# Optimization experiments

Measured on AMD Instinct MI355X. Metric: run time of the kernel, lower is better.

The kernel has to match this reference:

```python
import jax, jax.numpy as jnp
import numpy as np


def setup_inputs() -> dict:
    key = jax.random.key(0)
    ks = jax.random.split(key, 32)
    B, S, H, E, Vs, T = 32, 400, 512, 300, 200, 32
    EN, V = 50000, 50200
    rn = lambda k, shape, s=0.05: jax.random.normal(k, shape, jnp.float32) * s
    return {
        'encoder_hidden': rn(ks[0], (B, S, 2 * H), 1.0),
        'hidden0': rn(ks[1], (B, H), 1.0),
        'user_embed': rn(ks[2], (B, E), 1.0),
        'W_embed': rn(ks[3], (EN, E), 1.0),
        'W_ih': rn(ks[4], (3 * H, E)), 'W_hh': rn(ks[5], (3 * H, H)),
        'b_ih': rn(ks[6], (3 * H,)), 'b_hh': rn(ks[7], (3 * H,)),
        'Wk_c': rn(ks[8], (2 * H, H)), 'bk_c': rn(ks[9], (H,)),
        'Wq_c': rn(ks[10], (H, H)), 'bq_c': rn(ks[11], (H,)),
        'we_c': rn(ks[12], (H,)), 'be_c': rn(ks[13], (1,)),
        'Wk_u': rn(ks[14], (E, H)), 'bk_u': rn(ks[15], (H,)),
        'Wq_u': rn(ks[16], (H, H)), 'bq_u': rn(ks[17], (H,)),
        'we_u': rn(ks[18], (H,)), 'be_u': rn(ks[19], (1,)),
        'Wc': rn(ks[20], (3 * H + 2 * E, H)),
        'Wg': rn(ks[21], (3 * H + E,)), 'bg': rn(ks[22], (1,)),
        'Wgen': rn(ks[23], (H, EN)),
        'src_mask': jnp.ones((B, S), jnp.int32),
        'tgt_': jax.random.randint(ks[24], (B, T), 0, EN),
        'specific_vocab': jax.random.randint(ks[25], (B, Vs), 0, EN),
        'vocab_size': V,
    }


def reference(encoder_hidden, hidden0, user_embed, W_embed, W_ih, W_hh, b_ih, b_hh,
              Wk_c, bk_c, Wq_c, bq_c, we_c, be_c, Wk_u, bk_u, Wq_u, bq_u, we_u, be_u,
              Wc, Wg, bg, Wgen, src_mask, tgt_, specific_vocab, vocab_size):
    B, T = tgt_.shape
    # teacher forcing: prev token embed, step 0 uses <s> token id 1
    tgt_embed = W_embed[tgt_]                                  # [B,T,E]
    init_embed = jnp.broadcast_to(W_embed[1], (B, 1, W_embed.shape[1]))
    prev = jnp.concatenate([init_embed, tgt_embed[:, :T - 1]], axis=1)
    xs = jnp.swapaxes(prev, 0, 1)                              # [T,B,E]

    user_vocab_emb = W_embed[specific_vocab]                   # [B,Vs,E]
    proj_key_c = encoder_hidden @ Wk_c + bk_c                  # [B,S,H]
    proj_key_u = user_vocab_emb @ Wk_u + bk_u                  # [B,Vs,H]
    mask = src_mask != 0
    batch_idx = jnp.arange(B)[:, None]

    def gru_cell(h, x):
        gi = x @ W_ih.T + b_ih
        gh = h @ W_hh.T + b_hh
        i_r, i_z, i_n = jnp.split(gi, 3, axis=-1)
        h_r, h_z, h_n = jnp.split(gh, 3, axis=-1)
        r = jax.nn.sigmoid(i_r + h_r)
        z = jax.nn.sigmoid(i_z + h_z)
        n = jnp.tanh(i_n + r * h_n)
        return (1.0 - z) * n + z * h

    def step(h, x):
        h = gru_cell(h, x)                                     # [B,H]
        q = h
        # Bahdanau attention over encoder states
        sc = jnp.tanh((q @ Wq_c + bq_c)[:, None, :] + proj_key_c) @ we_c + be_c  # [B,S]
        sc = jnp.where(mask, sc, -1e9)
        ac = jax.nn.softmax(sc, axis=-1)
        ctx_c = jnp.einsum('bs,bsd->bd', ac, encoder_hidden)   # [B,2H]
        # Bahdanau attention over user-specific vocab embeddings
        su = jnp.tanh((q @ Wq_u + bq_u)[:, None, :] + proj_key_u) @ we_u + be_u  # [B,Vs]
        au = jax.nn.softmax(su, axis=-1)
        ctx_u = jnp.einsum('bv,bve->be', au, user_vocab_emb)   # [B,E]
        ch = jnp.tanh(jnp.concatenate([q, ctx_c, ctx_u, user_embed], axis=-1) @ Wc)
        gen_prob = jax.nn.softmax(ch @ Wgen, axis=-1)          # [B,embed_num]
        gen_prob = jnp.pad(gen_prob, ((0, 0), (0, vocab_size - gen_prob.shape[-1])))
        copy_prob = jnp.zeros((B, vocab_size), gen_prob.dtype).at[batch_idx, specific_vocab].add(au)
        copy_p = jax.nn.sigmoid(jnp.concatenate([ctx_c, q, ctx_u], axis=-1) @ Wg + bg[0])[:, None]
        mix = copy_p * copy_prob + (1.0 - copy_p) * gen_prob   # [B,vocab]
        return h, mix

    _, probs = jax.lax.scan(step, hidden0, xs)                 # [T,B,V]
    return jnp.swapaxes(probs, 0, 1)                           # [B,T,V]
```

## Files before the change

### kernel.cpp

```cpp
#include <hip/hip_runtime.h>


typedef __attribute__((ext_vector_type(8))) short short8;
typedef __attribute__((ext_vector_type(4))) float f32x4;
typedef unsigned short us;

#define SCW (-2.8853900817779268f)

__device__ __forceinline__ float bf2f(us u) {
  return __uint_as_float(((unsigned)u) << 16);
}
__device__ __forceinline__ us f2bf(float f) {
  unsigned x = __float_as_uint(f);
  unsigned r = x + 0x7fffu + ((x >> 16) & 1u);
  return (us)(r >> 16);
}
__device__ __forceinline__ float fsigmoid(float x) { return 1.f / (1.f + __expf(-x)); }
__device__ __forceinline__ float ftanh(float x) {
  float t = __expf(-2.f * fabsf(x));
  float r = (1.f - t) / (1.f + t);
  return x >= 0.f ? r : -r;
}
__device__ __forceinline__ float ftanh_fast(float x) {
  float u = exp2f(SCW * fabsf(x));
  float r = (1.f - u) * __builtin_amdgcn_rcpf(1.f + u);
  return copysignf(r, x);
}

struct PP {
  const float *enc, *hidden0, *Wk_c, *Wk_u, *Wq_c, *Wq_u, *Wc, *W_ih, *W_hh, *W_embed;
  const int *tgt, *sv;
  us *encb, *hball, *WkcT, *WkuT, *WqcuT, *WcT, *WihT, *WhhF, *xe, *uve;
};

__device__ void tcast_job(const float* __restrict__ src, us* __restrict__ dst,
                          int R, int C, int Rpad, int x, int y, float scale,
                          int lt, float* tb) {
  int tx = lt & 31, ty = lt >> 5;
  int c0 = x * 32, r0 = y * 32;
#pragma unroll
  for (int i = 0; i < 4; ++i) {
    int r = r0 + ty + i * 8, c = c0 + tx;
    tb[(ty + i * 8) * 33 + tx] = (r < R && c < C) ? src[(size_t)r * C + c] : 0.f;
  }
  __syncthreads();
#pragma unroll
  for (int i = 0; i < 4; ++i) {
    int c = c0 + ty + i * 8, rr = r0 + tx;
    if (c < C && rr < Rpad)
      dst[(size_t)c * Rpad + rr] = f2bf(scale * tb[tx * 33 + ty + i * 8]);
  }
}

__global__ __launch_bounds__(256) void k_prep(PP P) {
  __shared__ float tb[32 * 33];
  const int bid = blockIdx.x, tid = threadIdx.x;
  if (bid < 1024) {
    for (int i = bid * 256 + tid; i < 3276800; i += 1024 * 256) {
      float4 v = ((const float4*)P.enc)[i];
// ... 54 lines not shown
}

__global__ __launch_bounds__(256) void k_tcastX(const float* __restrict__ src0,
                                                us* __restrict__ dst0,
                                                int R, int C, int Rpad,
                                                size_t srcB, size_t dstB) {
  __shared__ float tile[32 * 33];
  const float* src = src0 + (size_t)blockIdx.z * srcB;
  us* dst = dst0 + (size_t)blockIdx.z * dstB;
  tcast_job(src, dst, R, C, Rpad, blockIdx.x, blockIdx.y, 1.f, threadIdx.x, tile);
}
__global__ __launch_bounds__(256) void k_tcastXb(const us* __restrict__ src0,
                                                 us* __restrict__ dst0,
                                                 int R, int C, int Rpad,
                                                 size_t srcB, size_t dstB) {
  __shared__ us tile[32][33];
  const us* src = src0 + (size_t)blockIdx.z * srcB;
  us* dst = dst0 + (size_t)blockIdx.z * dstB;
  int c0 = blockIdx.x * 32, r0 = blockIdx.y * 32;
  int tx = threadIdx.x & 31, ty = threadIdx.x >> 5;
#pragma unroll
  for (int i = 0; i < 4; ++i) {
    int r = r0 + ty + i * 8, c = c0 + tx;
    tile[ty + i * 8][tx] = (r < R && c < C) ? src[(size_t)r * C + c] : (us)0;
  }
  __syncthreads();
#pragma unroll
  for (int i = 0; i < 4; ++i) {
    int c = c0 + ty + i * 8, rr = r0 + tx;
    if (c < C && rr < Rpad) dst[(size_t)c * Rpad + rr] = tile[tx][ty + i * 8];
  }
}

template <int MODE>
__global__ __launch_bounds__(512) void gemm_bt(const us* __restrict__ A,
                                               const us* __restrict__ BT,
                                               int M, int N, int K, int Ntiles,
                                               const float* __restrict__ bias,
                                               float bscale,
                                               us* __restrict__ outB,
                                               float* __restrict__ outF,
                                               float* __restrict__ rowsum) {
  __shared__ us sh[12288];
  __shared__ float rs[256];
  us* As = sh;
  us* Bs = sh + 8192;
  const int tid = threadIdx.x;
  const int lane = tid & 63, wid = tid >> 6;
  const int wr = wid >> 1, wc = wid & 1;
  const int bx = blockIdx.x;
  const int mt = bx / Ntiles, nt = bx - mt * Ntiles;
  const int m0 = mt * 256, n0 = nt * 128;
  f32x4 acc[4][4] = {};
  for (int kk = 0; kk < K; kk += 32) {
    uint4 av0, av1, bv;
    {
      int c = tid, row = c >> 2, c8 = (c & 3) * 8;
      av0 = *(const uint4*)(A + (size_t)(m0 + row) * K + kk + c8);
      c = tid + 512; row = c >> 2; c8 = (c & 3) * 8;
      av1 = *(const uint4*)(A + (size_t)(m0 + row) * K + kk + c8);
      c = tid; row = c >> 2; c8 = (c & 3) * 8;
      int nr = n0 + row; if (nr > N - 1) nr = N - 1;
      bv = *(const uint4*)(BT + (size_t)nr * K + kk + c8);
    }
    __syncthreads();
    ((uint4*)As)[tid] = av0;
    ((uint4*)As)[tid + 512] = av1;
    ((uint4*)Bs)[tid] = bv;
    __syncthreads();
    short8 af[4], bfr[4];
#pragma unroll
    for (int m = 0; m < 4; ++m)
      af[m] = *(const short8*)(As + (wr * 64 + m * 16 + (lane & 15)) * 32 + (lane >> 4) * 8);
#pragma unroll
    for (int n = 0; n < 4; ++n)
      bfr[n] = *(const short8*)(Bs + (wc * 64 + n * 16 + (lane & 15)) * 32 + (lane >> 4) * 8);
#pragma unroll
    for (int m = 0; m < 4; ++m)
#pragma unroll
      for (int n = 0; n < 4; ++n)
        acc[m][n] = __builtin_amdgcn_mfma_f32_16x16x32_bf16(af[m], bfr[n], acc[m][n], 0, 0, 0);
  }
  if (MODE == 0) {
#pragma unroll
// ... 78 lines not shown
    ((uint4*)As)[tid] = av;
    ((uint4*)Bs)[tid * 2] = bv0;
    ((uint4*)Bs)[tid * 2 + 1] = bv1;
    __syncthreads();
    short8 af[4], bf0, bf1;
#pragma unroll
    for (int m = 0; m < 4; ++m)
      af[m] = *(const short8*)(As + (m * 16 + (lane & 15)) * 32 + (lane >> 4) * 8);
    bf0 = *(const short8*)(Bs + ((w * 2 + 0) * 16 + (lane & 15)) * 32 + (lane >> 4) * 8);
    bf1 = *(const short8*)(Bs + ((w * 2 + 1) * 16 + (lane & 15)) * 32 + (lane >> 4) * 8);
#pragma unroll
    for (int m = 0; m < 4; ++m) {
      acc[m][0] = __builtin_amdgcn_mfma_f32_16x16x32_bf16(af[m], bf0, acc[m][0], 0, 0, 0);
      acc[m][1] = __builtin_amdgcn_mfma_f32_16x16x32_bf16(af[m], bf1, acc[m][1], 0, 0, 0);
    }
  }
#pragma unroll
  for (int m = 0; m < 4; ++m)
#pragma unroll
    for (int q = 0; q < 2; ++q)
#pragma unroll
      for (int reg = 0; reg < 4; ++reg) {
        int r = m0 + m * 16 + (lane >> 4) * 4 + reg;
        int c = n0 + (w * 2 + q) * 16 + (lane & 15);
        float v = acc[m][q][reg];
        if (MODE == 0) v += bscale * bias[c];
        else v = ftanh_fast(v);
        outB[(size_t)r * N + c] = f2bf(v);
      }
}

struct FP {
  const us* frag; const us* gib; const float* bhh; const float* hidden0;
  us* hball; float* hfall; int* arrive;
  const us* xe; const us* WihT; const float* bih; us* gibout;
  const us* encb; const us* WkcT; const float* bkc; us* pkc;
  const us* uve; const us* WkuT; const float* bku; us* pku;
  const float* Wgen; us* WT;
  const float* enc; us* encTp;
  us* uveTp;
};

__device__ void gru_body(const FP& P, int q, int tid, char* pool) {
  us* hs = (us*)pool;
  float* gh = (float*)(pool + 32768);
  const int lane = tid & 63, w = tid >> 6;
  short8 bfr[16];
  {
    const us* fb = P.frag + (((size_t)(q * 12 + w) * 16) * 64 + lane) * 8;
#pragma unroll
    for (int kt = 0; kt < 16; ++kt) bfr[kt] = *(const short8*)(fb + (size_t)kt * 512);
  }
  float hprev[3];
#pragma unroll
  for (int s = 0; s < 3; ++s) {
    int i = tid + s * 768;
    if (i < 2048) {
      int b = i >> 6, jj = i & 63;
      hprev[s] = P.hidden0[b * 512 + q * 64 + jj];
    }
  }
  if (tid == 0) {
    while (__hip_atomic_load(P.arrive + 32, __ATOMIC_ACQUIRE,
                             __HIP_MEMORY_SCOPE_AGENT) < 48) {
      __builtin_amdgcn_s_sleep(1);
    }
  }
  __syncthreads();
  const int sw = (lane & 7) << 3;
  for (int t = 0; t < 32; ++t) {
    if (t > 0) {
      if (tid == 0) {
        while (__hip_atomic_load(P.arrive + (t - 1), __ATOMIC_ACQUIRE,
                                 __HIP_MEMORY_SCOPE_AGENT) < 8) {
          __builtin_amdgcn_s_sleep(1);
        }
      }
      __syncthreads();
    }
    const us* hp = P.hball + (size_t)t * 16384;
    for (int i = tid; i < 2048; i += 768)
      ((uint4*)hs)[i ^ ((i >> 6) & 7)] = *(const uint4*)(hp + i * 8);
    __syncthreads();
    f32x4 acc0 = {}, acc1 = {};
#pragma unroll
    for (int kt = 0; kt < 16; ++kt) {
      int base0 = ((lane & 15) * 512 + kt * 32 + (lane >> 4) * 8) ^ sw;
      int base1 = (((lane & 15) + 16) * 512 + kt * 32 + (lane >> 4) * 8) ^ sw;
      short8 a0 = *(const short8*)(hs + base0);
      short8 a1 = *(const short8*)(hs + base1);
      acc0 = __builtin_amdgcn_mfma_f32_16x16x32_bf16(a0, bfr[kt], acc0, 0, 0, 0);
      acc1 = __builtin_amdgcn_mfma_f32_16x16x32_bf16(a1, bfr[kt], acc1, 0, 0, 0);
    }
    {
      int col = w * 16 + (lane & 15);
#pragma unroll
      for (int reg = 0; reg < 4; ++reg) {
        gh[col * 33 + ((lane >> 4) * 4 + reg)] = acc0[reg];
        gh[col * 33 + (16 + (lane >> 4) * 4 + reg)] = acc1[reg];
      }
    }
    __syncthreads();
    us* hbn = P.hball + (size_t)(t + 1) * 16384;
    float* hfn = P.hfall + (size_t)t * 16384;
#pragma unroll
    for (int s = 0; s < 3; ++s) {
      int i = tid + s * 768;
      if (i < 2048) {
        int b = i >> 6, jj = i & 63, j = q * 64 + jj;
        float g0 = gh[jj * 33 + b] + P.bhh[j];
        float g1 = gh[(64 + jj) * 33 + b] + P.bhh[512 + j];
        float g2 = gh[(128 + jj) * 33 + b] + P.bhh[1024 + j];
        size_t gbase = (size_t)(t * 32 + b) * 1536;
        float r_ = fsigmoid(bf2f(P.gib[gbase + j]) + g0);
        float z_ = fsigmoid(bf2f(P.gib[gbase + 512 + j]) + g1);
        float n_ = ftanh(bf2f(P.gib[gbase + 1024 + j]) + r_ * g2);
        float hv = (1.f - z_) * n_ + z_ * hprev[s];
        hprev[s] = hv;
        hbn[b * 512 + j] = f2bf(hv);
        hfn[b * 512 + j] = hv;
      }
    }
    __syncthreads();
    if (tid == 0)
      __hip_atomic_fetch_add(P.arrive + t, 1, __ATOMIC_RELEASE,
                             __HIP_MEMORY_SCOPE_AGENT);
  }
}

__device__ void gemm0_body(const us* A, const us* BT, int N, int K,
                           int mt, int nt, const float* bias, float bscale,
                           us* outB, int tid, char* pool) {
  us* As = (us*)pool;
  us* Bs = (us*)(pool + 16384);
  const bool act = tid < 512;
  const int lane = tid & 63, wid = (tid >> 6) & 7;
  const int wr = wid >> 1, wc = wid & 1;
  const int m0 = mt * 256, n0 = nt * 128;
  f32x4 acc[4][4] = {};
  for (int kk = 0; kk < K; kk += 32) {
    uint4 av0 = {0, 0, 0, 0}, av1 = {0, 0, 0, 0}, bv = {0, 0, 0, 0};
    if (act) {
      int c = tid, row = c >> 2, c8 = (c & 3) * 8;
      av0 = *(const uint4*)(A + (size_t)(m0 + row) * K + kk + c8);
      av1 = *(const uint4*)(A + (size_t)(m0 + 128 + row) * K + kk + c8);
      int nr = n0 + row; if (nr > N - 1) nr = N - 1;
      bv = *(const uint4*)(BT + (size_t)nr * K + kk + c8);
    }
    __syncthreads();
    if (act) {
      ((uint4*)As)[tid] = av0;
      ((uint4*)As)[tid + 512] = av1;
      ((uint4*)Bs)[tid] = bv;
    }
    __syncthreads();
    if (act) {
      short8 af[4], bfr[4];
#pragma unroll
      for (int m = 0; m < 4; ++m)
        af[m] = *(const short8*)(As + (wr * 64 + m * 16 + (lane & 15)) * 32 + (lane >> 4) * 8);
#pragma unroll
      for (int n = 0; n < 4; ++n)
        bfr[n] = *(const short8*)(Bs + (wc * 64 + n * 16 + (lane & 15)) * 32 + (lane >> 4) * 8);
#pragma unroll
      for (int m = 0; m < 4; ++m)
#pragma unroll
        for (int n = 0; n < 4; ++n)
          acc[m][n] = __builtin_amdgcn_mfma_f32_16x16x32_bf16(af[m], bfr[n], acc[m][n], 0, 0, 0);
    }
  }
  if (act) {
#pragma unroll
    for (int m = 0; m < 4; ++m)
#pragma unroll
      for (int n = 0; n < 4; ++n)
#pragma unroll
        for (int reg = 0; reg < 4; ++reg) {
          int r = m0 + wr * 64 + m * 16 + (lane >> 4) * 4 + reg;
          int c = n0 + wc * 64 + n * 16 + (lane & 15);
          outB[(size_t)r * N + c] = f2bf(acc[m][n][reg] + bscale * bias[c]);
        }
  }
}

__global__ __launch_bounds__(768, 1) void k_fat(FP P) {
  __shared__ char pool[98304];
  const int bid = blockIdx.x, tid = threadIdx.x;
  if (bid < 8) { gru_body(P, bid, tid, pool); return; }
  if (bid < 56) {
    int j = bid - 8;
    gemm0_body(P.xe, P.WihT, 1536, 320, j / 12, j % 12, P.bih, 1.f, P.gibout, tid, pool);
    __syncthreads();
    if (tid == 0)
      __hip_atomic_fetch_add(P.arrive + 32, 1, __ATOMIC_RELEASE,
                             __HIP_MEMORY_SCOPE_AGENT);
    return;
  }
  if (bid < 256) {
    int j = bid - 56;
    gemm0_body(P.encb, P.WkcT, 512, 1024, j >> 2, j & 3, P.bkc, SCW, P.pkc, tid, pool);
    return;
  }
  if (bid < 356) {
    int j = bid - 256;
    gemm0_body(P.uve, P.WkuT, 512, 320, j >> 2, j & 3, P.bku, SCW, P.pku, tid, pool);
    return;
  }
  const int g = tid >> 8, lt = tid & 255;
  const int tx = lt & 31, ty = lt >> 5;
  float* tb = (float*)(pool + g * 4224);
  if (bid < 878) {
    int base = (bid - 356) * 3 + g;
    for (int it = 0; it < 16; ++it) {
      int sub = base + it * 1566;
      bool valid = sub < 25008;
      int x = valid ? sub % 1563 : 0, y = valid ? sub / 1563 : 0;
      int c0 = x * 32, r0 = y * 32;
      if (valid) {
#pragma unroll
        for (int i = 0; i < 4; ++i) {
          int r = r0 + ty + i * 8, c = c0 + tx;
          tb[(ty + i * 8) * 33 + tx] =
              (c < 50000) ? P.Wgen[(size_t)r * 50000 + c] : 0.f;
        }
      }
      __syncthreads();
      if (valid) {
#pragma unroll
        for (int i = 0; i < 4; ++i) {
          int c = c0 + ty + i * 8;
          if (c < 50000)
            P.WT[(size_t)c * 512 + r0 + tx] = f2bf(tb[tx * 33 + ty + i * 8]);
        }
      }
      __syncthreads();
    }
    return;
  }
  if (bid < 1156) {
    int base = (bid - 878) * 3 + g;
    for (int it = 0; it < 16; ++it) {
      int sub = base + it * 834;
      bool valid = sub < 13312;
      int x = sub & 31, rem = sub >> 5;
      int y = rem % 13, z = rem / 13;
      const float* src = P.enc + (size_t)z * 409600;
      us* dst = P.encTp + (size_t)z * 425984;
      int c0 = x * 32, r0 = y * 32;
      if (valid) {
#pragma unroll
        for (int i = 0; i < 4; ++i) {
          int r = r0 + ty + i * 8, c = c0 + tx;
          tb[(ty + i * 8) * 33 + tx] = (r < 400) ? src[(size_t)r * 1024 + c] : 0.f;
        }
      }
      __syncthreads();
      if (valid) {
#pragma unroll
        for (int i = 0; i < 4; ++i) {
          int c = c0 + ty + i * 8, rr = r0 + tx;
          if (rr < 416) dst[(size_t)c * 416 + rr] = f2bf(tb[tx * 33 + ty + i * 8]);
        }
      }
      __syncthreads();
    }
    return;
  }
  {
    us* tbu = (us*)tb;
    int base = (bid - 1156) * 3 + g;
    for (int it = 0; it < 16; ++it) {
      int sub = base + it * 141;
      bool valid = sub < 2240;
      int x = sub % 10, rem = sub / 10;
      int y = rem % 7, z = rem / 7;
      const us* src = P.uve + (size_t)z * 64000;
      us* dst = P.uveTp + (size_t)z * 71680;
      int c0 = x * 32, r0 = y * 32;
      if (valid) {
#pragma unroll
        for (int i = 0; i < 4; ++i) {
          int r = r0 + ty + i * 8, c = c0 + tx;
          tbu[(ty + i * 8) * 33 + tx] = (r < 200) ? src[(size_t)r * 320 + c] : (us)0;
        }
      }
      __syncthreads();
      if (valid) {
#pragma unroll
        for (int i = 0; i < 4; ++i) {
          int c = c0 + ty + i * 8, rr = r0 + tx;
          if (rr < 224) dst[(size_t)c * 224 + rr] = tbu[tx * 33 + ty + i * 8];
        }
      }
      __syncthreads();
    }
  }
}

__global__ __launch_bounds__(256) void k_scores(const us* __restrict__ Qall,
                                                const us* __restrict__ pkc,
                                                const us* __restrict__ pku,
                                                const float* __restrict__ wec,
                                                const float* __restrict__ bec,
// ... 11 lines not shown
    int r = bid % 50;
    s0 = (r >> 1) * 16; th = r & 1; qoff = 0; S = 400;
  } else {
    int j = bid - 1600;
    b = j / 26;
    int r = j % 26;
    s0 = (r >> 1) * 16; th = r & 1; qoff = 512; S = 200;
  }
  for (int i = threadIdx.x; i < 1024; i += 256) {
    int tt = th * 16 + (i >> 6), c8 = (i & 63) * 8;
    ((uint4*)q)[i] = *(const uint4*)(Qall + (size_t)(tt * 32 + b) * 1024 + qoff + c8);
  }
  const int w = threadIdx.x >> 6, lane = threadIdx.x & 63;
  const int d0 = lane * 8;
  const float* we = enc ? wec : weu;
  float wef[8];
  {
    float4 w0 = *(const float4*)(we + d0);
    float4 w1 = *(const float4*)(we + d0 + 4);
    wef[0] = w0.x; wef[1] = w0.y; wef[2] = w0.z; wef[3] = w0.w;
    wef[4] = w1.x; wef[5] = w1.y; wef[6] = w1.z; wef[7] = w1.w;
  }
  const float bias = enc ? bec[0] : beu[0];
  float pkf[4][8];
  int ss[4], validv[4], maskedv[4];
#pragma unroll
  for (int si = 0; si < 4; ++si) {
    int s = s0 + w * 4 + si;
    validv[si] = (s < S);
    int sc = validv[si] ? s : (S - 1);
    ss[si] = sc;
    const us* pk = enc ? pkc + ((size_t)b * 400 + sc) * 512
                       : pku + ((size_t)b * 200 + sc) * 512;
    uint4 pkv = *(const uint4*)(pk + d0);
    pkf[si][0] = bf2f((us)(pkv.x & 0xffff)); pkf[si][1] = bf2f((us)(pkv.x >> 16));
    pkf[si][2] = bf2f((us)(pkv.y & 0xffff)); pkf[si][3] = bf2f((us)(pkv.y >> 16));
    pkf[si][4] = bf2f((us)(pkv.z & 0xffff)); pkf[si][5] = bf2f((us)(pkv.z >> 16));
    pkf[si][6] = bf2f((us)(pkv.w & 0xffff)); pkf[si][7] = bf2f((us)(pkv.w >> 16));
    maskedv[si] = enc ? (src_mask[b * 400 + sc] == 0) : 0;
  }
  __syncthreads();
  for (int tl = 0; tl < 16; ++tl) {
    short8 qv = *(const short8*)(q + tl * 512 + d0);
    float qf[8];
#pragma unroll
    for (int d = 0; d < 8; ++d) qf[d] = bf2f((us)qv[d]);
#pragma unroll
    for (int si = 0; si < 4; ++si) {
      float a = 0.f;
#pragma unroll
      for (int d = 0; d < 8; ++d) {
        float x = qf[d] + pkf[si][d];
        float u = exp2f(-fabsf(x));
        float r2v = (1.f - u) * __builtin_amdgcn_rcpf(1.f + u);
        a = fmaf(copysignf(r2v, -x), wef[d], a);
      }
#pragma unroll
      for (int m = 1; m < 64; m <<= 1) a += __shfl_xor(a, m, 64);
      if (lane == 0 && validv[si]) {
        int t = th * 16 + tl;
        float v = a + bias;
        if (enc) sc_enc[(size_t)(t * 32 + b) * 400 + ss[si]] = maskedv[si] ? -1e9f : v;
        else sc_usr[(size_t)(t * 32 + b) * 200 + ss[si]] = v;
      }
    }
  }
}

__device__ __forceinline__ float bmax256(float v, float* r4, int tid) {
#pragma unroll
  for (int m = 1; m < 64; m <<= 1) v = fmaxf(v, __shfl_xor(v, m, 64));
  if ((tid & 63) == 0) r4[tid >> 6] = v;
  __syncthreads();
  float x = fmaxf(fmaxf(r4[0], r4[1]), fmaxf(r4[2], r4[3]));
  __syncthreads();
  return x;
}
__device__ __forceinline__ float bsum256(float v, float* r4, int tid) {
#pragma unroll
  for (int m = 1; m < 64; m <<= 1) v += __shfl_xor(v, m, 64);
  if ((tid & 63) == 0) r4[tid >> 6] = v;
  __syncthreads();
  float x = r4[0] + r4[1] + r4[2] + r4[3];
  __syncthreads();
  return x;
}

__global__ __launch_bounds__(256) void k_softmax(const float* __restrict__ sc_enc,
                                                 const float* __restrict__ sc_usr,
                                                 const float* __restrict__ bg,
                                                 us* __restrict__ AC,
                                                 us* __restrict__ AU,
                                                 float* __restrict__ aual,
                                                 float* __restrict__ cp_acc) {
  __shared__ float r4[4];
  int r = blockIdx.x, tid = threadIdx.x;
  if (r < 1024) {
    int t = r >> 5, b = r & 31;
    float v0 = (tid < 400) ? sc_enc[(size_t)r * 400 + tid] : -3e38f;
    float v1 = (tid + 256 < 400) ? sc_enc[(size_t)r * 400 + tid + 256] : -3e38f;
    float mx = bmax256(fmaxf(v0, v1), r4, tid);
    float e0 = (tid < 400) ? __expf(v0 - mx) : 0.f;
    float e1 = (tid + 256 < 400) ? __expf(v1 - mx) : 0.f;
    float inv = 1.f / bsum256(e0 + e1, r4, tid);
    us* ACb = AC + (size_t)(b * 32 + t) * 416;
    if (tid < 400) ACb[tid] = f2bf(e0 * inv);
    int s2 = tid + 256;
    if (s2 < 400) ACb[s2] = f2bf(e1 * inv);
    else if (s2 < 416) ACb[s2] = 0;
    if (tid == 0) cp_acc[r] = bg[0];
  } else {
    int rr = r - 1024;
    int t = rr >> 5, b = rr & 31;
    float v0 = (tid < 200) ? sc_usr[(size_t)rr * 200 + tid] : -3e38f;
    float mx = bmax256(v0, r4, tid);
    float e0 = (tid < 200) ? __expf(v0 - mx) : 0.f;
    float inv = 1.f / bsum256(e0, r4, tid);
    us* AUb = AU + (size_t)(b * 32 + t) * 224;
    if (tid < 200) {
      float a = e0 * inv;
      AUb[tid] = f2bf(a);
      aual[(size_t)rr * 200 + tid] = a;
    } else if (tid < 224) {
      AUb[tid] = 0;
    }
  }
}

__global__ __launch_bounds__(256) void k_ctx(const us* __restrict__ A,
                                             const us* __restrict__ BT,
                                             const float* __restrict__ Wg,
                                             us* __restrict__ catall,
                                             float* __restrict__ cp_acc,
                                             int N, int Kp, int catOff, int wgOff,
                                             int Nvalid) {
  __shared__ us As[32 * 32];
  __shared__ us Bs[128 * 32];
  __shared__ float gaccs[32];
  const int b = blockIdx.y, n0 = blockIdx.x * 128;
  const us* Ab = A + (size_t)b * 32 * Kp;
  const us* Bb = BT + (size_t)b * N * Kp;
  const int tid = threadIdx.x, lane = tid & 63, w = tid >> 6;
  if (tid < 32) gaccs[tid] = 0.f;
  f32x4 acc[2][2] = {};
  for (int kk = 0; kk < Kp; kk += 32) {
    uint4 av, bv0, bv1;
    if (tid < 128) av = *(const uint4*)(Ab + (size_t)(tid >> 2) * Kp + kk + (tid & 3) * 8);
    {
      int i0 = tid * 2, row0 = i0 >> 2, c0 = (i0 & 3) * 8;
      int i1 = tid * 2 + 1, row1 = i1 >> 2, c1 = (i1 & 3) * 8;
      int nr0 = n0 + row0; if (nr0 > N - 1) nr0 = N - 1;
      int nr1 = n0 + row1; if (nr1 > N - 1) nr1 = N - 1;
      bv0 = *(const uint4*)(Bb + (size_t)nr0 * Kp + kk + c0);
      bv1 = *(const uint4*)(Bb + (size_t)nr1 * Kp + kk + c1);
    }
    __syncthreads();
    if (tid < 128) ((uint4*)As)[tid] = av;
    ((uint4*)Bs)[tid * 2] = bv0;
    ((uint4*)Bs)[tid * 2 + 1] = bv1;
    __syncthreads();
    short8 a0 = *(const short8*)(As + ((lane & 15)) * 32 + (lane >> 4) * 8);
    short8 a1 = *(const short8*)(As + (16 + (lane & 15)) * 32 + (lane >> 4) * 8);
#pragma unroll
    for (int qq = 0; qq < 2; ++qq) {
      short8 bf_ = *(const short8*)(Bs + ((w * 2 + qq) * 16 + (lane & 15)) * 32 + (lane >> 4) * 8);
      acc[0][qq] = __builtin_amdgcn_mfma_f32_16x16x32_bf16(a0, bf_, acc[0][qq], 0, 0, 0);
      acc[1][qq] = __builtin_amdgcn_mfma_f32_16x16x32_bf16(a1, bf_, acc[1][qq], 0, 0, 0);
    }
  }
#pragma unroll
  for (int mt = 0; mt < 2; ++mt)
#pragma unroll
    for (int qq = 0; qq < 2; ++qq)
#pragma unroll
      for (int reg = 0; reg < 4; ++reg) {
        int t_ = mt * 16 + (lane >> 4) * 4 + reg;
        int c = n0 + (w * 2 + qq) * 16 + (lane & 15);
        if (c < Nvalid) {
          float v = acc[mt][qq][reg];
          catall[(size_t)(t_ * 32 + b) * 2144 + catOff + c] = f2bf(v);
          atomicAdd(&gaccs[t_], v * Wg[wgOff + c]);
        }
      }
  __syncthreads();
  if (tid < 32) atomicAdd(&cp_acc[tid * 32 + b], gaccs[tid]);
}

__global__ __launch_bounds__(256) void k_catgate(const us* __restrict__ hball,
                                                 const float* __restrict__ hfall,
                                                 const float* __restrict__ ue,
                                                 const float* __restrict__ Wg,
                                                 const float* __restrict__ cp_acc,
                                                 us* __restrict__ catall,
                                                 float* __restrict__ cp_all) {
  __shared__ float r4[4];
  int r = blockIdx.x, tid = threadIdx.x;
  int t = r >> 5, b = r & 31;
  us* row = catall + (size_t)r * 2144;
  const us* hb = hball + (size_t)(t + 1) * 16384 + b * 512;
  row[tid] = hb[tid];
  row[256 + tid] = hb[256 + tid];
  float gp = 0.f;
  for (int i = tid; i < 512; i += 256)
    gp += hfall[(size_t)t * 16384 + b * 512 + i] * Wg[1024 + i];
  for (int i = tid; i < 308; i += 256)
    row[1836 + i] = (i < 300) ? f2bf(ue[b * 300 + i]) : (us)0;
  float gtot = bsum256(gp, r4, tid);
  if (tid == 0) cp_all[r] = fsigmoid(gtot + cp_acc[r]);
}

__global__ __launch_bounds__(256) void k_finalize(float* __restrict__ out,
                                                  const float* __restrict__ rowsum,
                                                  const float* __restrict__ cp_all,
                                                  const float* __restrict__ au_all,
                                                  const int* __restrict__ sv) {
  int r = blockIdx.x;
  int t = threadIdx.x;
  int b = r & 31, tt = r >> 5;
  float cp = cp_all[r];
  float scale = (1.f - cp) / rowsum[r];
  float* base = out + (size_t)(b * 32 + tt) * 50200;
  float4* b4 = (float4*)base;
  for (int i = t; i < 12550; i += 256) {
    if (i < 12500) {
      float4 v = b4[i];
      v.x *= scale; v.y *= scale; v.z *= scale; v.w *= scale;
      b4[i] = v;
    } else {
      b4[i] = make_float4(0.f, 0.f, 0.f, 0.f);
    }
  }
  __syncthreads();
  if (t < 200) {
    int idx = sv[b * 200 + t];
    atomicAdd(base + idx, cp * au_all[(size_t)r * 200 + t]);
  }
}

__global__ __launch_bounds__(256) void k_finalize2(const us* __restrict__ expb,
                                                   const float* __restrict__ rowsum,
                                                   const float* __restrict__ cp_all,
                                                   const float* __restrict__ au_all,
                                                   const int* __restrict__ sv,
                                                   float* __restrict__ out) {
  int r = blockIdx.x;
  int t = threadIdx.x;
  int b = r & 31, tt = r >> 5;
  float cp = cp_all[r];
  float scale = (1.f - cp) / rowsum[r];
  size_t obase = (size_t)(b * 32 + tt) * 50200;
  const uint4* eb = (const uint4*)(expb + obase);
  float4* ob = (float4*)(out + obase);
  for (int i = t; i < 6275; i += 256) {
    float4 o0, o1;
    if (i < 6250) {
      uint4 ev = eb[i];
      o0.x = bf2f((us)(ev.x & 0xffff)) * scale; o0.y = bf2f((us)(ev.x >> 16)) * scale;
      o0.z = bf2f((us)(ev.y & 0xffff)) * scale; o0.w = bf2f((us)(ev.y >> 16)) * scale;
      o1.x = bf2f((us)(ev.z & 0xffff)) * scale; o1.y = bf2f((us)(ev.z >> 16)) * scale;
      o1.z = bf2f((us)(ev.w & 0xffff)) * scale; o1.w = bf2f((us)(ev.w >> 16)) * scale;
    } else {
      o0 = make_float4(0.f, 0.f, 0.f, 0.f);
      o1 = o0;
    }
    ob[i * 2] = o0;
    ob[i * 2 + 1] = o1;
  }
  __syncthreads();
  if (t < 200) {
    int idx = sv[b * 200 + t];
    atomicAdd(out + obase + idx, cp * au_all[(size_t)r * 200 + t]);
  }
}


extern "C" void kernel_launch(void* const* d_in, const int* in_sizes, int n_in,
                              void* d_out, int out_size, void* d_ws, size_t ws_size,
                              hipStream_t stream) {
  (void)in_sizes; (void)n_in; (void)out_size;
  const float* enc = (const float*)d_in[0];
  const float* hidden0 = (const float*)d_in[1];
// ... 12 lines not shown
  const float* Wk_u = (const float*)d_in[14];
  const float* bk_u = (const float*)d_in[15];
  const float* Wq_u = (const float*)d_in[16];
  const float* bq_u = (const float*)d_in[17];
  const float* we_u = (const float*)d_in[18];
  const float* be_u = (const float*)d_in[19];
  const float* Wc = (const float*)d_in[20];
  const float* Wg = (const float*)d_in[21];
  const float* bg = (const float*)d_in[22];
  const float* Wgen = (const float*)d_in[23];
  const int* src_mask = (const int*)d_in[24];
  const int* tgt = (const int*)d_in[25];
  const int* sv = (const int*)d_in[26];
  float* out = (float*)d_out;

  char* base = (char*)d_ws;
  size_t off = 0;
  auto take = [&](size_t bytes) {
    char* p = base + off;
    off += (bytes + 255) & ~(size_t)255;
    return p;
  };
  us* WT = (us*)take(50000ull * 512 * 2);
  char* R0 = take(32ull * 1024 * 416 * 2);
  us* encb = (us*)R0;
  char* RCD = take(12800ull * 512 * 2 + 6400ull * 512 * 2);
  us* pkc = (us*)RCD;
  us* pku = (us*)(RCD + 12800ull * 512 * 2);
  us* AC = (us*)RCD;
  us* AU = (us*)(RCD + 860160);
  float* aual = (float*)(RCD + 860160 + 458752);
  us* catall = (us*)(RCD + 860160 + 458752 + 819200);
  us* chb = (us*)(RCD + 860160 + 458752 + 819200 + 4390912);
  char* RU = take(6400ull * 320 * 2);
  us* uve = (us*)RU;
  float* sc_enc = (float*)RU;
  float* sc_usr = (float*)(RU + 1024ull * 400 * 4);
  us* uveTp = (us*)take(32ull * 320 * 224 * 2);
  char* RG = take(2700000);
  us* WkcT = (us*)RG;
  us* WihT = (us*)(RG + 1048576);
  us* xe = (us*)(RG + 1048576 + 983040);
  us* Qall = (us*)RG;
  us* WkuT = (us*)take(512ull * 320 * 2);
  us* WqcuT = (us*)take(1024ull * 512 * 2);
  us* WcT = (us*)take(512ull * 2144 * 2);
  us* WhhF = (us*)take(1536ull * 512 * 2);
  us* gib = (us*)take(1024ull * 1536 * 2);
  us* hball = (us*)take(33ull * 16384 * 2);
  float* hfall = (float*)take(32ull * 16384 * 4);
  float* bqcu = (float*)take(1024 * 4);
  float* cp_acc = (float*)take(1024 * 4);
  float* cp_all = (float*)take(1024 * 4);
  float* rsum = (float*)take(1024 * 4);
  int* arrive = (int*)take(33 * 4);
  size_t expb_bytes = 1024ull * 50200 * 2;
  bool big_ws = (ws_size >= off + expb_bytes + 256);
  us* expb = big_ws ? (us*)take(expb_bytes) : nullptr;
  us* encTp = big_ws ? expb : (us*)R0;

  hipMemcpyAsync(bqcu, bq_c, 512 * 4, hipMemcpyDeviceToDevice, stream);
  hipMemcpyAsync(bqcu + 512, bq_u, 512 * 4, hipMemcpyDeviceToDevice, stream);
  hipMemsetAsync(rsum, 0, 1024 * 4, stream);
  hipMemsetAsync(arrive, 0, 33 * 4, stream);

  PP pp;
  pp.enc = enc; pp.hidden0 = hidden0; pp.Wk_c = Wk_c; pp.Wk_u = Wk_u;
  pp.Wq_c = Wq_c; pp.Wq_u = Wq_u; pp.Wc = Wc; pp.W_ih = W_ih; pp.W_hh = W_hh;
  pp.W_embed = W_embed; pp.tgt = tgt; pp.sv = sv;
  pp.encb = encb; pp.hball = hball; pp.WkcT = WkcT; pp.WkuT = WkuT;
  pp.WqcuT = WqcuT; pp.WcT = WcT; pp.WihT = WihT; pp.WhhF = WhhF;
  pp.xe = xe; pp.uve = uve;
  k_prep<<<5920, 256, 0, stream>>>(pp);

  FP fp;
  fp.frag = WhhF; fp.gib = gib; fp.bhh = b_hh; fp.hidden0 = hidden0;
  fp.hball = hball; fp.hfall = hfall; fp.arrive = arrive;
  fp.xe = xe; fp.WihT = WihT; fp.bih = b_ih; fp.gibout = gib;
  fp.encb = encb; fp.WkcT = WkcT; fp.bkc = bk_c; fp.pkc = pkc;
  fp.uve = uve; fp.WkuT = WkuT; fp.bku = bk_u; fp.pku = pku;
  fp.Wgen = Wgen; fp.WT = WT; fp.enc = enc; fp.encTp = encTp; fp.uveTp = uveTp;

  if (big_ws) {
    k_fat<<<1203, 768, 0, stream>>>(fp);
  } else {
    k_tcastX<<<dim3(1563, 16, 1), 256, 0, stream>>>(Wgen, WT, 512, 50000, 512, 0, 0);
    gemm_bt<0><<<200, 512, 0, stream>>>(encb, WkcT, 12800, 512, 1024, 4, bk_c, SCW,
                                        pkc, nullptr, nullptr);
    gemm_bt<0><<<100, 512, 0, stream>>>(uve, WkuT, 6400, 512, 320, 4, bk_u, SCW,
                                        pku, nullptr, nullptr);
    k_tcastX<<<dim3(32, 13, 32), 256, 0, stream>>>(enc, encTp, 400, 1024, 416,
                                                   400ull * 1024, 1024ull * 416);
    k_tcastXb<<<dim3(10, 7, 32), 256, 0, stream>>>(uve, uveTp, 200, 320, 224,
                                                   200ull * 320, 320ull * 224);
    k_fat<<<56, 768, 0, stream>>>(fp);
  }

  gemm_med<0><<<128, 256, 0, stream>>>(hball + 16384, WqcuT, 1024, 1024, 512, 8,
                                       bqcu, SCW, Qall);
  k_scores<<<2432, 256, 0, stream>>>(Qall, pkc, pku, we_c, be_c, we_u, be_u,
                                     src_mask, sc_enc, sc_usr);
  k_softmax<<<2048, 256, 0, stream>>>(sc_enc, sc_usr, bg, AC, AU, aual, cp_acc);
  k_ctx<<<dim3(8, 32), 256, 0, stream>>>(AC, encTp, Wg, catall, cp_acc,
                                         1024, 416, 512, 0, 1024);
  k_ctx<<<dim3(3, 32), 256, 0, stream>>>(AU, uveTp, Wg, catall, cp_acc,
                                         320, 224, 1536, 1536, 300);
  k_catgate<<<1024, 256, 0, stream>>>(hball, hfall, user_embed, Wg, cp_acc,
                                      catall, cp_all);
  gemm_med<2><<<64, 256, 0, stream>>>(catall, WcT, 1024, 512, 2144, 4, nullptr,
                                      1.f, chb);
  if (big_ws) {
    gemm_bt<3><<<4 * 391, 512, 0, stream>>>(chb, WT, 1024, 50000, 512, 391, nullptr,
                                            1.f, expb, nullptr, rsum);
    k_finalize2<<<1024, 256, 0, stream>>>(expb, rsum, cp_all, aual, sv, out);
  } else {
    gemm_bt<1><<<4 * 391, 512, 0, stream>>>(chb, WT, 1024, 50000, 512, 391, nullptr,
                                            1.f, nullptr, out, rsum);
    k_finalize<<<1024, 256, 0, stream>>>(out, rsum, cp_all, aual, sv);
  }
}
```

Before: 689.5 us.

## Move input-gate GEMM out of fat kernel, fuse softmax/catgate/ctx launches, reorder vocab GEMM tiles

The GRU input-projection GEMM moves out of the persistent fat kernel into a separate gemm_med launch, so the GRU blocks no longer spin on an arrival counter. The fp32 hidden-state history (hfall) is dropped. The gate dot product over h now runs inside a fused softmax kernel that also fills catall rows, and the sigmoid for copy_p moves into the finalize kernels. The two k_ctx launches merge into one, and the vocab GEMM blocks are remapped so consecutive blocks share the same N tile, which should improve L2 reuse of WT. This removes launches and an fp32 buffer, but the GRU recurrence can no longer overlap with the input GEMM.

```diff
diff --git a/kernel.cpp b/kernel.cpp
--- a/kernel.cpp
+++ b/kernel.cpp
@@ -25,6 +25,12 @@
   float u = exp2f(SCW * fabsf(x));
   float r = (1.f - u) * __builtin_amdgcn_rcpf(1.f + u);
   return copysignf(r, x);
+}
+__device__ __forceinline__ void unpack8(uint4 v, float* f) {
+  f[0] = bf2f((us)(v.x & 0xffff)); f[1] = bf2f((us)(v.x >> 16));
+  f[2] = bf2f((us)(v.y & 0xffff)); f[3] = bf2f((us)(v.y >> 16));
+  f[4] = bf2f((us)(v.z & 0xffff)); f[5] = bf2f((us)(v.z >> 16));
+  f[6] = bf2f((us)(v.w & 0xffff)); f[7] = bf2f((us)(v.w >> 16));
 }
 
 struct PP {
@@ -145,7 +151,7 @@
   }
 }
 
-template <int MODE>
+template <int MODE, bool NM = false>
 __global__ __launch_bounds__(512) void gemm_bt(const us* __restrict__ A,
                                                const us* __restrict__ BT,
                                                int M, int N, int K, int Ntiles,
@@ -162,7 +168,9 @@
   const int lane = tid & 63, wid = tid >> 6;
   const int wr = wid >> 1, wc = wid & 1;
   const int bx = blockIdx.x;
-  const int mt = bx / Ntiles, nt = bx - mt * Ntiles;
+  int mt, nt;
+  if (NM) { mt = bx & 3; nt = bx >> 2; }
+  else { mt = bx / Ntiles; nt = bx - mt * Ntiles; }
   const int m0 = mt * 256, n0 = nt * 128;
   f32x4 acc[4][4] = {};
   for (int kk = 0; kk < K; kk += 32) {
@@ -307,8 +315,7 @@
 
 struct FP {
   const us* frag; const us* gib; const float* bhh; const float* hidden0;
-  us* hball; float* hfall; int* arrive;
-  const us* xe; const us* WihT; const float* bih; us* gibout;
+  us* hball; int* arrive;
   const us* encb; const us* WkcT; const float* bkc; us* pkc;
   const us* uve; const us* WkuT; const float* bku; us* pku;
   const float* Wgen; us* WT;
@@ -335,13 +342,6 @@
       hprev[s] = P.hidden0[b * 512 + q * 64 + jj];
     }
   }
-  if (tid == 0) {
-    while (__hip_atomic_load(P.arrive + 32, __ATOMIC_ACQUIRE,
-                             __HIP_MEMORY_SCOPE_AGENT) < 48) {
-      __builtin_amdgcn_s_sleep(1);
-    }
-  }
-  __syncthreads();
   const int sw = (lane & 7) << 3;
   for (int t = 0; t < 32; ++t) {
     if (t > 0) {
@@ -377,7 +377,6 @@
     }
     __syncthreads();
     us* hbn = P.hball + (size_t)(t + 1) * 16384;
-    float* hfn = P.hfall + (size_t)t * 16384;
 #pragma unroll
     for (int s = 0; s < 3; ++s) {
       int i = tid + s * 768;
@@ -393,7 +392,6 @@
         float hv = (1.f - z_) * n_ + z_ * hprev[s];
         hprev[s] = hv;
         hbn[b * 512 + j] = f2bf(hv);
-        hfn[b * 512 + j] = hv;
       }
     }
     __syncthreads();
@@ -459,33 +457,24 @@
 }
 
 __global__ __launch_bounds__(768, 1) void k_fat(FP P) {
-  __shared__ char pool[98304];
+  __shared__ char pool[58368];
   const int bid = blockIdx.x, tid = threadIdx.x;
   if (bid < 8) { gru_body(P, bid, tid, pool); return; }
-  if (bid < 56) {
+  if (bid < 208) {
     int j = bid - 8;
-    gemm0_body(P.xe, P.WihT, 1536, 320, j / 12, j % 12, P.bih, 1.f, P.gibout, tid, pool);
-    __syncthreads();
-    if (tid == 0)
-      __hip_atomic_fetch_add(P.arrive + 32, 1, __ATOMIC_RELEASE,
-                             __HIP_MEMORY_SCOPE_AGENT);
-    return;
-  }
-  if (bid < 256) {
-    int j = bid - 56;
     gemm0_body(P.encb, P.WkcT, 512, 1024, j >> 2, j & 3, P.bkc, SCW, P.pkc, tid, pool);
     return;
   }
-  if (bid < 356) {
-    int j = bid - 256;
+  if (bid < 308) {
+    int j = bid - 208;
     gemm0_body(P.uve, P.WkuT, 512, 320, j >> 2, j & 3, P.bku, SCW, P.pku, tid, pool);
     return;
   }
   const int g = tid >> 8, lt = tid & 255;
   const int tx = lt & 31, ty = lt >> 5;
   float* tb = (float*)(pool + g * 4224);
-  if (bid < 878) {
-    int base = (bid - 356) * 3 + g;
+  if (bid < 830) {
+    int base = (bid - 308) * 3 + g;
     for (int it = 0; it < 16; ++it) {
       int sub = base + it * 1566;
       bool valid = sub < 25008;
@@ -512,8 +501,8 @@
     }
     return;
   }
-  if (bid < 1156) {
-    int base = (bid - 878) * 3 + g;
+  if (bid < 1108) {
+    int base = (bid - 830) * 3 + g;
     for (int it = 0; it < 16; ++it) {
       int sub = base + it * 834;
       bool valid = sub < 13312;
@@ -543,7 +532,7 @@
   }
   {
     us* tbu = (us*)tb;
-    int base = (bid - 1156) * 3 + g;
+    int base = (bid - 1108) * 3 + g;
     for (int it = 0; it < 16; ++it) {
       int sub = base + it * 141;
       bool valid = sub < 2240;
@@ -621,11 +610,7 @@
     ss[si] = sc;
     const us* pk = enc ? pkc + ((size_t)b * 400 + sc) * 512
                        : pku + ((size_t)b * 200 + sc) * 512;
-    uint4 pkv = *(const uint4*)(pk + d0);
-    pkf[si][0] = bf2f((us)(pkv.x & 0xffff)); pkf[si][1] = bf2f((us)(pkv.x >> 16));
-    pkf[si][2] = bf2f((us)(pkv.y & 0xffff)); pkf[si][3] = bf2f((us)(pkv.y >> 16));
-    pkf[si][4] = bf2f((us)(pkv.z & 0xffff)); pkf[si][5] = bf2f((us)(pkv.z >> 16));
-    pkf[si][6] = bf2f((us)(pkv.w & 0xffff)); pkf[si][7] = bf2f((us)(pkv.w >> 16));
+    unpack8(*(const uint4*)(pk + d0), pkf[si]);
     maskedv[si] = enc ? (src_mask[b * 400 + sc] == 0) : 0;
   }
   __syncthreads();
@@ -675,19 +660,22 @@
   return x;
 }
 
-__global__ __launch_bounds__(256) void k_softmax(const float* __restrict__ sc_enc,
-                                                 const float* __restrict__ sc_usr,
-                                                 const float* __restrict__ bg,
-                                                 us* __restrict__ AC,
-                                                 us* __restrict__ AU,
-                                                 float* __restrict__ aual,
-                                                 float* __restrict__ cp_acc) {
+__global__ __launch_bounds__(256) void k_soft2(const float* __restrict__ sc_enc,
+                                               const float* __restrict__ sc_usr,
+                                               us* __restrict__ AC,
+                                               us* __restrict__ AU,
+                                               float* __restrict__ aual,
+                                               float* __restrict__ cp_acc,
+                                               const us* __restrict__ hball,
+                                               const float* __restrict__ ue,
+                                               const float* __restrict__ Wg,
+                                               us* __restrict__ catall) {
   __shared__ float r4[4];
-  int r = blockIdx.x, tid = threadIdx.x;
-  if (r < 1024) {
-    int t = r >> 5, b = r & 31;
-    float v0 = (tid < 400) ? sc_enc[(size_t)r * 400 + tid] : -3e38f;
-    float v1 = (tid + 256 < 400) ? sc_enc[(size_t)r * 400 + tid + 256] : -3e38f;
+  int bid = blockIdx.x, tid = threadIdx.x;
+  if (bid < 1024) {
+    int t = bid >> 5, b = bid & 31;
+    float v0 = (tid < 400) ? sc_enc[(size_t)bid * 400 + tid] : -3e38f;
+    float v1 = (tid + 256 < 400) ? sc_enc[(size_t)bid * 400 + tid + 256] : -3e38f;
     float mx = bmax256(fmaxf(v0, v1), r4, tid);
     float e0 = (tid < 400) ? __expf(v0 - mx) : 0.f;
     float e1 = (tid + 256 < 400) ? __expf(v1 - mx) : 0.f;
@@ -697,9 +685,8 @@
     int s2 = tid + 256;
     if (s2 < 400) ACb[s2] = f2bf(e1 * inv);
     else if (s2 < 416) ACb[s2] = 0;
-    if (tid == 0) cp_acc[r] = bg[0];
-  } else {
-    int rr = r - 1024;
+  } else if (bid < 2048) {
+    int rr = bid - 1024;
     int t = rr >> 5, b = rr & 31;
     float v0 = (tid < 200) ? sc_usr[(size_t)rr * 200 + tid] : -3e38f;
     float mx = bmax256(v0, r4, tid);
@@ -713,23 +700,39 @@
     } else if (tid < 224) {
       AUb[tid] = 0;
     }
-  }
-}
-
-__global__ __launch_bounds__(256) void k_ctx(const us* __restrict__ A,
-                                             const us* __restrict__ BT,
-                                             const float* __restrict__ Wg,
-                                             us* __restrict__ catall,
-                                             float* __restrict__ cp_acc,
-                                             int N, int Kp, int catOff, int wgOff,
-                                             int Nvalid) {
-  __shared__ us As[32 * 32];
-  __shared__ us Bs[128 * 32];
-  __shared__ float gaccs[32];
-  const int b = blockIdx.y, n0 = blockIdx.x * 128;
-  const us* Ab = A + (size_t)b * 32 * Kp;
-  const us* Bb = BT + (size_t)b * N * Kp;
-  const int tid = threadIdx.x, lane = tid & 63, w = tid >> 6;
+  } else if (bid < 2304) {
+    int w = tid >> 6, lane = tid & 63;
+    int row = (bid - 2048) * 4 + w;
+    int t = row >> 5, b = row & 31;
+    us* rowp = catall + (size_t)row * 2144;
+    const us* hb = hball + (size_t)(t + 1) * 16384 + b * 512;
+    *(uint4*)(rowp + lane * 8) = *(const uint4*)(hb + lane * 8);
+    for (int i = lane; i < 308; i += 64)
+      rowp[1836 + i] = (i < 300) ? f2bf(ue[b * 300 + i]) : (us)0;
+  } else {
+    int w = tid >> 6, lane = tid & 63, d0 = lane * 8;
+#pragma unroll
+    for (int k = 0; k < 2; ++k) {
+      int row = (bid - 2304) * 8 + w * 2 + k;
+      int t = row >> 5, b = row & 31;
+      float hv[8];
+      unpack8(*(const uint4*)(hball + (size_t)(t + 1) * 16384 + b * 512 + d0), hv);
+      float4 g0 = *(const float4*)(Wg + 1024 + d0);
+      float4 g1 = *(const float4*)(Wg + 1024 + d0 + 4);
+      float a = hv[0] * g0.x + hv[1] * g0.y + hv[2] * g0.z + hv[3] * g0.w +
+                hv[4] * g1.x + hv[5] * g1.y + hv[6] * g1.z + hv[7] * g1.w;
+#pragma unroll
+      for (int m = 1; m < 64; m <<= 1) a += __shfl_xor(a, m, 64);
+      if (lane == 0) atomicAdd(&cp_acc[row], a);
+    }
+  }
+}
+
+__device__ void ctx_core(const us* Ab, const us* Bb, const float* Wg,
+                         us* catall, float* cp_acc, int b, int N, int Kp,
+                         int n0, int catOff, int wgOff, int Nvalid, int tid,
+                         us* As, us* Bs, float* gaccs) {
+  const int lane = tid & 63, w = tid >> 6;
   if (tid < 32) gaccs[tid] = 0.f;
   f32x4 acc[2][2] = {};
   for (int kk = 0; kk < Kp; kk += 32) {
@@ -775,38 +778,38 @@
   if (tid < 32) atomicAdd(&cp_acc[tid * 32 + b], gaccs[tid]);
 }
 
-__global__ __launch_bounds__(256) void k_catgate(const us* __restrict__ hball,
-                                                 const float* __restrict__ hfall,
-                                                 const float* __restrict__ ue,
-                                                 const float* __restrict__ Wg,
-                                                 const float* __restrict__ cp_acc,
-                                                 us* __restrict__ catall,
-                                                 float* __restrict__ cp_all) {
-  __shared__ float r4[4];
-  int r = blockIdx.x, tid = threadIdx.x;
-  int t = r >> 5, b = r & 31;
-  us* row = catall + (size_t)r * 2144;
-  const us* hb = hball + (size_t)(t + 1) * 16384 + b * 512;
-  row[tid] = hb[tid];
-  row[256 + tid] = hb[256 + tid];
-  float gp = 0.f;
-  for (int i = tid; i < 512; i += 256)
-    gp += hfall[(size_t)t * 16384 + b * 512 + i] * Wg[1024 + i];
-  for (int i = tid; i < 308; i += 256)
-    row[1836 + i] = (i < 300) ? f2bf(ue[b * 300 + i]) : (us)0;
-  float gtot = bsum256(gp, r4, tid);
-  if (tid == 0) cp_all[r] = fsigmoid(gtot + cp_acc[r]);
+__global__ __launch_bounds__(256) void k_ctx2(const us* __restrict__ AC,
+                                              const us* __restrict__ encTp,
+                                              const us* __restrict__ AU,
+                                              const us* __restrict__ uveTp,
+                                              const float* __restrict__ Wg,
+                                              us* __restrict__ catall,
+                                              float* __restrict__ cp_acc) {
+  __shared__ us As[32 * 32];
+  __shared__ us Bs[128 * 32];
+  __shared__ float gaccs[32];
+  int bid = blockIdx.x, tid = threadIdx.x;
+  if (bid < 256) {
+    int b = bid >> 3, nt = bid & 7;
+    ctx_core(AC + (size_t)b * 32 * 416, encTp + (size_t)b * 1024 * 416, Wg,
+             catall, cp_acc, b, 1024, 416, nt * 128, 512, 0, 1024, tid, As, Bs, gaccs);
+  } else {
+    int j = bid - 256;
+    int b = j / 3, nt = j % 3;
+    ctx_core(AU + (size_t)b * 32 * 224, uveTp + (size_t)b * 320 * 224, Wg,
+             catall, cp_acc, b, 320, 224, nt * 128, 1536, 1536, 300, tid, As, Bs, gaccs);
+  }
 }
 
 __global__ __launch_bounds__(256) void k_finalize(float* __restrict__ out,
                                                   const float* __restrict__ rowsum,
-                                                  const float* __restrict__ cp_all,
+                                                  const float* __restrict__ cp_acc,
+                                                  const float* __restrict__ bg,
                                                   const float* __restrict__ au_all,
                                                   const int* __restrict__ sv) {
-  int r = blockIdx.x;
-  int t = threadIdx.x;
+  int r = blockIdx.x, t = threadIdx.x;
   int b = r & 31, tt = r >> 5;
-  float cp = cp_all[r];
+  float cp = fsigmoid(cp_acc[r] + bg[0]);
   float scale = (1.f - cp) / rowsum[r];
   float* base = out + (size_t)(b * 32 + tt) * 50200;
   float4* b4 = (float4*)base;
@@ -828,14 +831,14 @@
 
 __global__ __launch_bounds__(256) void k_finalize2(const us* __restrict__ expb,
                                                    const float* __restrict__ rowsum,
-                                                   const float* __restrict__ cp_all,
+                                                   const float* __restrict__ cp_acc,
+                                                   const float* __restrict__ bg,
                                                    const float* __restrict__ au_all,
                                                    const int* __restrict__ sv,
                                                    float* __restrict__ out) {
-  int r = blockIdx.x;
-  int t = threadIdx.x;
+  int r = blockIdx.x, t = threadIdx.x;
   int b = r & 31, tt = r >> 5;
-  float cp = cp_all[r];
+  float cp = fsigmoid(cp_acc[r] + bg[0]);
   float scale = (1.f - cp) / rowsum[r];
   size_t obase = (size_t)(b * 32 + tt) * 50200;
   const uint4* eb = (const uint4*)(expb + obase);
@@ -914,28 +917,25 @@
   float* aual = (float*)(RCD + 860160 + 458752);
   us* catall = (us*)(RCD + 860160 + 458752 + 819200);
   us* chb = (us*)(RCD + 860160 + 458752 + 819200 + 4390912);
-  char* RU = take(6400ull * 320 * 2);
-  us* uve = (us*)RU;
-  float* sc_enc = (float*)RU;
-  float* sc_usr = (float*)(RU + 1024ull * 400 * 4);
+  us* uve = (us*)take(6400ull * 320 * 2);
   us* uveTp = (us*)take(32ull * 320 * 224 * 2);
   char* RG = take(2700000);
   us* WkcT = (us*)RG;
   us* WihT = (us*)(RG + 1048576);
   us* xe = (us*)(RG + 1048576 + 983040);
-  us* Qall = (us*)RG;
   us* WkuT = (us*)take(512ull * 320 * 2);
   us* WqcuT = (us*)take(1024ull * 512 * 2);
   us* WcT = (us*)take(512ull * 2144 * 2);
   us* WhhF = (us*)take(1536ull * 512 * 2);
   us* gib = (us*)take(1024ull * 1536 * 2);
   us* hball = (us*)take(33ull * 16384 * 2);
-  float* hfall = (float*)take(32ull * 16384 * 4);
+  us* Qall = (us*)take(1024ull * 1024 * 2);
+  float* sc_enc = (float*)take(1024ull * 400 * 4);
+  float* sc_usr = (float*)take(1024ull * 200 * 4);
   float* bqcu = (float*)take(1024 * 4);
   float* cp_acc = (float*)take(1024 * 4);
-  float* cp_all = (float*)take(1024 * 4);
   float* rsum = (float*)take(1024 * 4);
-  int* arrive = (int*)take(33 * 4);
+  int* arrive = (int*)take(32 * 4);
   size_t expb_bytes = 1024ull * 50200 * 2;
   bool big_ws = (ws_size >= off + expb_bytes + 256);
   us* expb = big_ws ? (us*)take(expb_bytes) : nullptr;
@@ -944,7 +944,8 @@
   hipMemcpyAsync(bqcu, bq_c, 512 * 4, hipMemcpyDeviceToDevice, stream);
   hipMemcpyAsync(bqcu + 512, bq_u, 512 * 4, hipMemcpyDeviceToDevice, stream);
   hipMemsetAsync(rsum, 0, 1024 * 4, stream);
-  hipMemsetAsync(arrive, 0, 33 * 4, stream);
+  hipMemsetAsync(cp_acc, 0, 1024 * 4, stream);
+  hipMemsetAsync(arrive, 0, 32 * 4, stream);
 
   PP pp;
   pp.enc = enc; pp.hidden0 = hidden0; pp.Wk_c = Wk_c; pp.Wk_u = Wk_u;
@@ -954,17 +955,17 @@
   pp.WqcuT = WqcuT; pp.WcT = WcT; pp.WihT = WihT; pp.WhhF = WhhF;
   pp.xe = xe; pp.uve = uve;
   k_prep<<<5920, 256, 0, stream>>>(pp);
+  gemm_med<0><<<192, 256, 0, stream>>>(xe, WihT, 1024, 1536, 320, 12, b_ih, 1.f, gib);
 
   FP fp;
   fp.frag = WhhF; fp.gib = gib; fp.bhh = b_hh; fp.hidden0 = hidden0;
-  fp.hball = hball; fp.hfall = hfall; fp.arrive = arrive;
-  fp.xe = xe; fp.WihT = WihT; fp.bih = b_ih; fp.gibout = gib;
+  fp.hball = hball; fp.arrive = arrive;
   fp.encb = encb; fp.WkcT = WkcT; fp.bkc = bk_c; fp.pkc = pkc;
   fp.uve = uve; fp.WkuT = WkuT; fp.bku = bk_u; fp.pku = pku;
   fp.Wgen = Wgen; fp.WT = WT; fp.enc = enc; fp.encTp = encTp; fp.uveTp = uveTp;
 
   if (big_ws) {
-    k_fat<<<1203, 768, 0, stream>>>(fp);
+    k_fat<<<1155, 768, 0, stream>>>(fp);
   } else {
     k_tcastX<<<dim3(1563, 16, 1), 256, 0, stream>>>(Wgen, WT, 512, 50000, 512, 0, 0);
     gemm_bt<0><<<200, 512, 0, stream>>>(encb, WkcT, 12800, 512, 1024, 4, bk_c, SCW,
@@ -975,29 +976,25 @@
                                                    400ull * 1024, 1024ull * 416);
     k_tcastXb<<<dim3(10, 7, 32), 256, 0, stream>>>(uve, uveTp, 200, 320, 224,
                                                    200ull * 320, 320ull * 224);
-    k_fat<<<56, 768, 0, stream>>>(fp);
+    k_fat<<<8, 768, 0, stream>>>(fp);
   }
 
   gemm_med<0><<<128, 256, 0, stream>>>(hball + 16384, WqcuT, 1024, 1024, 512, 8,
                                        bqcu, SCW, Qall);
   k_scores<<<2432, 256, 0, stream>>>(Qall, pkc, pku, we_c, be_c, we_u, be_u,
                                      src_mask, sc_enc, sc_usr);
-  k_softmax<<<2048, 256, 0, stream>>>(sc_enc, sc_usr, bg, AC, AU, aual, cp_acc);
-  k_ctx<<<dim3(8, 32), 256, 0, stream>>>(AC, encTp, Wg, catall, cp_acc,
-                                         1024, 416, 512, 0, 1024);
-  k_ctx<<<dim3(3, 32), 256, 0, stream>>>(AU, uveTp, Wg, catall, cp_acc,
-                                         320, 224, 1536, 1536, 300);
-  k_catgate<<<1024, 256, 0, stream>>>(hball, hfall, user_embed, Wg, cp_acc,
-                                      catall, cp_all);
+  k_soft2<<<2432, 256, 0, stream>>>(sc_enc, sc_usr, AC, AU, aual, cp_acc,
+                                    hball, user_embed, Wg, catall);
+  k_ctx2<<<352, 256, 0, stream>>>(AC, encTp, AU, uveTp, Wg, catall, cp_acc);
   gemm_med<2><<<64, 256, 0, stream>>>(catall, WcT, 1024, 512, 2144, 4, nullptr,
                                       1.f, chb);
   if (big_ws) {
-    gemm_bt<3><<<4 * 391, 512, 0, stream>>>(chb, WT, 1024, 50000, 512, 391, nullptr,
-                                            1.f, expb, nullptr, rsum);
-    k_finalize2<<<1024, 256, 0, stream>>>(expb, rsum, cp_all, aual, sv, out);
+    gemm_bt<3, true><<<4 * 391, 512, 0, stream>>>(chb, WT, 1024, 50000, 512, 391,
+                                                  nullptr, 1.f, expb, nullptr, rsum);
+    k_finalize2<<<1024, 256, 0, stream>>>(expb, rsum, cp_acc, bg, aual, sv, out);
   } else {
-    gemm_bt<1><<<4 * 391, 512, 0, stream>>>(chb, WT, 1024, 50000, 512, 391, nullptr,
-                                            1.f, nullptr, out, rsum);
-    k_finalize<<<1024, 256, 0, stream>>>(out, rsum, cp_all, aual, sv);
-  }
-}
+    gemm_bt<1, true><<<4 * 391, 512, 0, stream>>>(chb, WT, 1024, 50000, 512, 391,
+                                                  nullptr, 1.f, nullptr, out, rsum);
+    k_finalize<<<1024, 256, 0, stream>>>(out, rsum, cp_acc, bg, aual, sv);
+  }
+}
```

New measurement: 682.9 us. About the same (-0.9%).
